# Kernel tuning notes

Hardware: AMD Instinct MI355X
Metric: run time of the kernel (lower is better)

## Reference

```python
import jax, jax.numpy as jnp
import numpy as np

L, D, H, F, K = 2, 256, 8, 512, 9
M, G1, G2, NT = 4, 40, 40, 2048
DH = D // H
KPD = 3  # per-dim neighbour window; KPD**2 == K


def setup_inputs() -> dict:
    key = jax.random.key(0)
    ks = jax.random.split(key, 16)
    s = 0.02
    ax0 = jnp.linspace(-1.0, 1.0, G1)
    ax1 = jnp.linspace(-1.0, 1.0, G2)
    gx, gy = jnp.meshgrid(ax0, ax1, indexing='ij')
    xc = jnp.broadcast_to(jnp.stack([gx, gy], -1), (M, G1, G2, 2))  # regular grid coords
    zc = jax.random.normal(ks[0], (M, G1, G2, D), dtype=jnp.float32)
    xt = jax.random.uniform(ks[1], (M, NT, 2), minval=-1.0, maxval=1.0)
    zt = jax.random.normal(ks[2], (M, NT, D), dtype=jnp.float32)
    def n(k, shape):
        return jax.random.normal(k, shape, dtype=jnp.float32) * s
    def ln():
        return jnp.stack([jnp.ones((L, D)), jnp.zeros((L, D))], 1)  # [L, 2(gamma,beta), D]
    return dict(
        xc=xc, zc=zc, xt=xt, zt=zt,
        sa_wqkv=n(ks[3], (L, D, 3 * D)), sa_wo=n(ks[4], (L, D, D)),
        sa_ln1=ln(), sa_ln2=ln(),
        sa_w1=n(ks[5], (L, D, F)), sa_b1=jnp.zeros((L, F)),
        sa_w2=n(ks[6], (L, F, D)), sa_b2=jnp.zeros((L, D)),
        ca_wq=n(ks[7], (L, D, D)), ca_wkv=n(ks[8], (L, D, 2 * D)), ca_wo=n(ks[9], (L, D, D)),
        ca_lnq=ln(), ca_lnkv=ln(), ca_ln2=ln(),
        ca_w1=n(ks[10], (L, D, F)), ca_b1=jnp.zeros((L, F)),
        ca_w2=n(ks[11], (L, F, D)), ca_b2=jnp.zeros((L, D)),
    )


def _ln(x, p):
    mu = x.mean(-1, keepdims=True)
    var = ((x - mu) ** 2).mean(-1, keepdims=True)
    return (x - mu) * jax.lax.rsqrt(var + 1e-5) * p[0] + p[1]


def nearest_gridded_neighbours(xt, xc):
    """Separable per-dim nearest grid index + KPD x KPD window, clamped at borders.
    Returns flat neighbour indices [M, NT, K] and validity mask [M, NT, K]."""
    ax0 = xc[:, :, 0, 0]  # [M, G1] axis-0 coordinates
    ax1 = xc[:, 0, :, 1]  # [M, G2] axis-1 coordinates
    n0 = jnp.argmin(jnp.abs(xt[..., 0:1] - ax0[:, None, :]), -1)  # [M, NT]
    n1 = jnp.argmin(jnp.abs(xt[..., 1:2] - ax1[:, None, :]), -1)
    off = jnp.arange(KPD) - KPD // 2
    r0 = n0[..., None] + off  # [M, NT, KPD]
    r1 = n1[..., None] + off
    v0 = (r0 >= 0) & (r0 < G1)
    v1 = (r1 >= 0) & (r1 < G2)
    i0 = jnp.clip(r0, 0, G1 - 1)
    i1 = jnp.clip(r1, 0, G2 - 1)
    idx = (i0[:, :, :, None] * G2 + i1[:, :, None, :]).reshape(xt.shape[0], -1, K)
    mask = (v0[:, :, :, None] & v1[:, :, None, :]).reshape(xt.shape[0], -1, K)
    return idx, mask


def reference(xc, zc, xt, zt, sa_wqkv, sa_wo, sa_ln1, sa_ln2, sa_w1, sa_b1, sa_w2, sa_b2,
              ca_wq, ca_wkv, ca_wo, ca_lnq, ca_lnkv, ca_ln2, ca_w1, ca_b1, ca_w2, ca_b2):
    m = zc.shape[0]
    idx, mask = nearest_gridded_neighbours(xt, xc)
    zc = zc.reshape(m, G1 * G2, D)  # flatten_grid
    bidx = jnp.arange(m)[:, None, None]
    scale = 1.0 / np.sqrt(DH)
    for l in range(L):
        # --- MHSA over flattened grid (pre-norm transformer block) ---
        h = _ln(zc, sa_ln1[l])
        q, k, v = jnp.split(h @ sa_wqkv[l], 3, -1)
        q = q.reshape(m, -1, H, DH); k = k.reshape(m, -1, H, DH); v = v.reshape(m, -1, H, DH)
        att = jax.nn.softmax(jnp.einsum('bnhd,bkhd->bhnk', q, k) * scale, -1)
        o = jnp.einsum('bhnk,bkhd->bnhd', att, v).reshape(m, -1, D)
        zc = zc + o @ sa_wo[l]
        h = _ln(zc, sa_ln2[l])
        zc = zc + jax.nn.gelu(h @ sa_w1[l] + sa_b1[l]) @ sa_w2[l] + sa_b2[l]
        # --- per-target masked MHCA over K nearest grid tokens (MATH SDPA path) ---
        nzc = zc[bidx, idx]  # [M, NT, K, D] neighbour gather
        q = (_ln(zt, ca_lnq[l]) @ ca_wq[l]).reshape(m, NT, H, DH)
        kk, vv = jnp.split(_ln(nzc, ca_lnkv[l]) @ ca_wkv[l], 2, -1)
        kk = kk.reshape(m, NT, K, H, DH); vv = vv.reshape(m, NT, K, H, DH)
        s = jnp.einsum('bnhd,bnkhd->bnhk', q, kk) * scale
        s = jnp.where(mask[:, :, None, :], s, -1e30)
        att = jax.nn.softmax(s, -1)
        o = jnp.einsum('bnhk,bnkhd->bnhd', att, vv).reshape(m, NT, D)
        zt = zt + o @ ca_wo[l]
        h = _ln(zt, ca_ln2[l])
        zt = zt + jax.nn.gelu(h @ ca_w1[l] + ca_b1[l]) @ ca_w2[l] + ca_b2[l]
    return zt
```

## Files before the change

kernel.cpp:

```cpp
#include <hip/hip_runtime.h>
#include <math.h>

#define LAYERS 2
#define DMODEL 256
#define NHEAD  8
#define DHEAD  32
#define FF     512
#define KNB    9
#define MB     4
#define G1D    40
#define G2D    40
#define NTGT   2048
#define NCTX   1600
#define RC     (MB*NCTX)
#define RT     (MB*NTGT)
#define NSPLIT 4

typedef __attribute__((ext_vector_type(8))) short short8;
typedef __attribute__((ext_vector_type(4))) float f32x4;

#if __has_builtin(__builtin_amdgcn_exp2f)
#define EXP2(x) __builtin_amdgcn_exp2f(x)
#else
#define EXP2(x) exp2f(x)
#endif
#define L2E 1.4426950408889634f
#define ATTN_SCALE 0.17677669529663687f

#define ZC_OFF    0
#define HC_OFF    1638400
#define HT_OFF    (HC_OFF + 819200)
#define QKV_OFF   (HC_OFF + 2097152)
#define WT_OFF    (QKV_OFF + 3400000)
#define FB_OFF    (QKV_OFF + 4500000)
#define Q_OFF     (QKV_OFF + 4915200)
#define O_OFF     (Q_OFF + 2097152)
#define IDX_OFF   (O_OFF + 2097152)
#define MASK_OFF  (IDX_OFF + 73728)
#define OPART_OFF (MASK_OFF + 73728)
#define LB_OFF    (OPART_OFF + 3276800)
#define WS_FLOATS (LB_OFF + 204800)

#define WT_LAYER   1048576
#define WT_QKV     0
#define WT_WO      196608
#define WT_W1      262144
#define WT_W2      393216
#define WT_CWQ     524288
#define WT_CWKV    589824
#define WT_CWO     720896
#define WT_CW1     786432
#define WT_CW2     917504
#define FB_LAYER   2560
#define FB_QKV     0
#define FB_W1      768
#define FB_WKV     1280
#define FB_WQ      1792
#define FB_CW1     2048

static __device__ __forceinline__ float gelu_f(float x){
  float t = tanhf(0.7978845608028654f * (x + 0.044715f * x * x * x));
  return 0.5f * x * (1.0f + t);
}
static __device__ __forceinline__ unsigned int bf16_rne(float x){
  unsigned int u = __float_as_uint(x);
  return (u + 0x7fffu + ((u >> 16) & 1u)) >> 16;
}
static __device__ __forceinline__ unsigned int pack_bf16x2(float lo, float hi){
  return bf16_rne(lo) | (bf16_rne(hi) << 16);
}
static __device__ __forceinline__ float bfu(unsigned int u16){
  return __uint_as_float(u16 << 16);
}

struct TDesc { const float* src; const float* gamma; int dstoff; int K; int N; int nse; float nsc; };
struct TTable { TDesc e[18]; };

__global__ __launch_bounds__(256)
void wprep_kernel(TTable t, unsigned short* __restrict__ wt){
  TDesc d = t.e[blockIdx.z];
  int n0 = blockIdx.x * 32, k0 = blockIdx.y * 32;
  if (n0 >= d.N || k0 >= d.K) return;
  __shared__ float tile[32][33];
  int tx = threadIdx.x, ty = threadIdx.y;
  float csc = (n0 + tx < d.nse) ? d.nsc : 1.0f;
  #pragma unroll
  for (int j = 0; j < 4; j++){
    int k = k0 + ty * 4 + j;
    float v = d.src[(size_t)k * d.N + n0 + tx];
    if (d.gamma) v *= d.gamma[k];
    tile[ty * 4 + j][tx] = v * csc;
  }
  __syncthreads();
  #pragma unroll
  for (int j = 0; j < 4; j++)
    wt[(size_t)d.dstoff + (size_t)(n0 + ty * 4 + j) * d.K + k0 + tx] =
        (unsigned short)bf16_rne(tile[tx][ty * 4 + j]);
}

struct BDesc { const float* W; const float* beta; const float* base; int outoff; int N; int nse; float nsc; };
struct BTable { BDesc e[10]; };

__global__ __launch_bounds__(256)
void bfold_kernel(BTable t, float* __restrict__ fb){
  BDesc d = t.e[blockIdx.x];
  int n = blockIdx.y * 64 + (threadIdx.x >> 2);
  int q = threadIdx.x & 3;
  if (n >= d.N) return;
  float s = 0.f;
  #pragma unroll 4
  for (int k = q * 64; k < q * 64 + 64; k++)
    s += d.beta[k] * d.W[(size_t)k * d.N + n];
  s += __shfl_xor(s, 1);
  s += __shfl_xor(s, 2);
  if (q == 0){
    float r = s + (d.base ? d.base[n] : 0.f);
    if (n < d.nse) r *= d.nsc;
    fb[d.outoff + n] = r;
  }
}

__global__ void nn_idx_kernel(const float* __restrict__ xc, const float* __restrict__ xt,
                              int* __restrict__ idx, float* __restrict__ mask){
  int g = blockIdx.x * blockDim.x + threadIdx.x;
  if (g >= MB * NTGT) return;
  int m = g >> 11;
  float x0 = xt[(size_t)g * 2 + 0];
  float x1 = xt[(size_t)g * 2 + 1];
  const float* xcm = xc + (size_t)m * G1D * G2D * 2;
  int n0 = 0; float b0 = 1e30f;
  for (int i = 0; i < G1D; i++){
    float d = fabsf(x0 - xcm[i * (G2D * 2)]);
    if (d < b0){ b0 = d; n0 = i; }
  }
  int n1 = 0; float b1 = 1e30f;
  for (int j = 0; j < G2D; j++){
    float d = fabsf(x1 - xcm[j * 2 + 1]);
    if (d < b1){ b1 = d; n1 = j; }
  }
  #pragma unroll
  for (int a = 0; a < 3; a++){
    int r0 = n0 + a - 1;
    bool v0 = (r0 >= 0) && (r0 < G1D);
    int i0 = min(max(r0, 0), G1D - 1);
    #pragma unroll
    for (int b = 0; b < 3; b++){
      int r1 = n1 + b - 1;
      bool v1 = (r1 >= 0) && (r1 < G2D);
      int i1 = min(max(r1, 0), G2D - 1);
      idx [(size_t)g * KNB + a * 3 + b] = i0 * G2D + i1;
      mask[(size_t)g * KNB + a * 3 + b] = (v0 && v1) ? 1.0f : 0.0f;
    }
  }
}

__global__ __launch_bounds__(256)
void ln_norm(const float* __restrict__ x, unsigned short* __restrict__ y, int rows){
  int gw   = blockIdx.x * 4 + (threadIdx.x >> 6);
  int lane = threadIdx.x & 63;
  if (gw >= rows) return;
  const float* xr = x + (size_t)gw * DMODEL;
  int d0 = lane * 4;
  float4 xv = *(const float4*)(xr + d0);
  float s = xv.x + xv.y + xv.z + xv.w;
  #pragma unroll
  for (int off = 32; off > 0; off >>= 1) s += __shfl_xor(s, off);
  float mu = s * (1.0f / DMODEL);
  float dx0 = xv.x - mu, dx1 = xv.y - mu, dx2 = xv.z - mu, dx3 = xv.w - mu;
  float v = dx0*dx0 + dx1*dx1 + dx2*dx2 + dx3*dx3;
  #pragma unroll
  for (int off = 32; off > 0; off >>= 1) v += __shfl_xor(v, off);
  float rs = rsqrtf(v * (1.0f / DMODEL) + 1e-5f);
  uint2 w;
  w.x = pack_bf16x2(dx0 * rs, dx1 * rs);
  w.y = pack_bf16x2(dx2 * rs, dx3 * rs);
  *(uint2*)(y + (size_t)gw * DMODEL + d0) = w;
}

template<int ROWS>
static __device__ __forceinline__ void stage_glds(const unsigned short* __restrict__ src,
                                                  int Ksrc, unsigned short* lds,
                                                  int wave, int lane){
  #pragma unroll
  for (int j = 0; j < ROWS / 32; j++){
    int ublk = (j * 4 + wave) * 64;
    int u    = ublk + lane;
    int row  = u >> 3;
    int unit = (u & 7) ^ (row & 7);
    __builtin_amdgcn_global_load_lds(
        (const __attribute__((address_space(1))) void*)(src + (size_t)row * Ksrc + unit * 8),
        (__attribute__((address_space(3))) void*)(lds + (size_t)ublk * 8),
        16, 0, 0);
  }
}

template<int K, int MT, int NT>
__global__ __launch_bounds__(256)
void gemm_glds(const unsigned short* __restrict__ A, const unsigned short* __restrict__ Wt,
               const float* __restrict__ bias, const float* __restrict__ res,
               void* __restrict__ C, int N, int flags){
  const int MFR = MT / 32, NFR = NT / 32;
  __shared__ unsigned short Als[2][MT * 64];
  __shared__ unsigned short Bls[2][NT * 64];
  int tid = threadIdx.x;
  int wave = tid >> 6, lane = tid & 63;
  int wm = wave >> 1, wn = wave & 1;
  int l16 = lane & 15, grp = lane >> 4;
  int r0 = blockIdx.y * MT, c0 = blockIdx.x * NT;

  const unsigned short* Ag = A  + (size_t)r0 * K;
  const unsigned short* Bg = Wt + (size_t)c0 * K;
  const int nch = K >> 6;

  stage_glds<MT>(Ag, K, Als[0], wave, lane);
  stage_glds<NT>(Bg, K, Bls[0], wave, lane);

  f32x4 acc[MFR][NFR];
  #pragma unroll
  for (int m = 0; m < MFR; m++)
    #pragma unroll
    for (int n = 0; n < NFR; n++) acc[m][n] = (f32x4){0.f, 0.f, 0.f, 0.f};

  #pragma unroll
  for (int ch = 0; ch < nch; ch++){
    int b = ch & 1;
    __syncthreads();
    if (ch + 1 < nch){
      stage_glds<MT>(Ag + (ch + 1) * 64, K, Als[b ^ 1], wave, lane);
      stage_glds<NT>(Bg + (ch + 1) * 64, K, Bls[b ^ 1], wave, lane);
    }
    const unsigned short* Ab = Als[b];
    const unsigned short* Bb = Bls[b];
    #pragma unroll
    for (int kk = 0; kk < 2; kk++){
      short8 af[MFR], bfr[NFR];
      #pragma unroll
      for (int m = 0; m < MFR; m++){
        int row = wm * (MT / 2) + m * 16 + l16;
        int unit = (kk * 4 + grp) ^ (row & 7);
        af[m] = *(const short8*)(Ab + row * 64 + unit * 8);
      }
      #pragma unroll
      for (int n = 0; n < NFR; n++){
        int row = wn * (NT / 2) + n * 16 + l16;
        int unit = (kk * 4 + grp) ^ (row & 7);
        bfr[n] = *(const short8*)(Bb + row * 64 + unit * 8);
      }
      #pragma unroll
      for (int m = 0; m < MFR; m++)
        #pragma unroll
        for (int n = 0; n < NFR; n++)
          acc[m][n] = __builtin_amdgcn_mfma_f32_16x16x32_bf16(af[m], bfr[n], acc[m][n], 0, 0, 0);
    }
  }

  #pragma unroll
  for (int n = 0; n < NFR; n++){
    int gc = c0 + wn * (NT / 2) + n * 16 + l16;
    float bv = (flags & 1) ? bias[gc] : 0.f;
    #pragma unroll
    for (int m = 0; m < MFR; m++){
      int grb = r0 + wm * (MT / 2) + m * 16 + grp * 4;
      #pragma unroll
      for (int r = 0; r < 4; r++){
        float v = acc[m][n][r] + bv;
        if (flags & 2) v = gelu_f(v);
        if (flags & 4) v += res[(size_t)(grb + r) * N + gc];
        if (flags & 8) ((unsigned short*)C)[(size_t)(grb + r) * N + gc] = (unsigned short)bf16_rne(v);
        else           ((float*)C)[(size_t)(grb + r) * N + gc] = v;
      }
    }
  }
}

#define KSTR 40
#define VSTR 70
#define PSTR 72
__global__ __launch_bounds__(256)
void sa_attn_mfma(const unsigned short* __restrict__ qkv,
                  unsigned short* __restrict__ opart, float* __restrict__ lb){
  int mz = blockIdx.z;
  int m = mz & 3, split = mz >> 2;
  int h = blockIdx.y;
  int tid  = threadIdx.x;
  int wave = tid >> 6, lane = tid & 63;
  int qr = lane & 15, grp = lane >> 4;
  int q0 = blockIdx.x * 64 + wave * 16;

  int kt0 = split ? (7 + (split - 1) * 6) : 0;
  int kt1 = kt0 + (split ? 6 : 7);

  __shared__ unsigned short Kls[2][64 * KSTR];
  __shared__ unsigned short Vls[2][32 * VSTR];
  __shared__ unsigned short Pls[4][16 * PSTR];
  unsigned short* Pw = Pls[wave];

  short8 qf = *(const short8*)(qkv + ((size_t)(m * NCTX + q0 + qr)) * 768 + h * 32 + grp * 8);

  int skey = tid >> 2;
  int scol = (tid & 3) * 8;
  const unsigned short* kbase = qkv + (size_t)m * NCTX * 768 + 256 + h * 32 + scol;

  uint4 kreg = *(const uint4*)(kbase + (size_t)(kt0 * 64 + skey) * 768);
  uint4 vreg = *(const uint4*)(kbase + (size_t)(kt0 * 64 + skey) * 768 + 256);

  float lq = 0.0f;
  f32x4 acc0 = {0.f, 0.f, 0.f, 0.f};
  f32x4 acc1 = {0.f, 0.f, 0.f, 0.f};

  {
    *(uint4*)&Kls[0][skey * KSTR + scol] = kreg;
    unsigned int vv[4] = {vreg.x, vreg.y, vreg.z, vreg.w};
    #pragma unroll
    for (int j = 0; j < 4; j++){
      Vls[0][(scol + 2 * j    ) * VSTR + skey] = (unsigned short)(vv[j] & 0xffffu);
      Vls[0][(scol + 2 * j + 1) * VSTR + skey] = (unsigned short)(vv[j] >> 16);
    }
  }

  for (int kt = kt0; kt < kt1; kt++){
    int b = (kt - kt0) & 1;
    __syncthreads();
    if (kt + 1 < kt1){
      kreg = *(const uint4*)(kbase + (size_t)((kt + 1) * 64 + skey) * 768);
      vreg = *(const uint4*)(kbase + (size_t)((kt + 1) * 64 + skey) * 768 + 256);
    }

    f32x4 s0 = {0.f,0.f,0.f,0.f}, s1 = {0.f,0.f,0.f,0.f};
    f32x4 s2 = {0.f,0.f,0.f,0.f}, s3 = {0.f,0.f,0.f,0.f};
    {
      const short8 k0 = *(const short8*)&Kls[b][( 0 + qr) * KSTR + grp * 8];
      const short8 k1 = *(const short8*)&Kls[b][(16 + qr) * KSTR + grp * 8];
      const short8 k2 = *(const short8*)&Kls[b][(32 + qr) * KSTR + grp * 8];
      const short8 k3 = *(const short8*)&Kls[b][(48 + qr) * KSTR + grp * 8];
      s0 = __builtin_amdgcn_mfma_f32_16x16x32_bf16(k0, qf, s0, 0, 0, 0);
      s1 = __builtin_amdgcn_mfma_f32_16x16x32_bf16(k1, qf, s1, 0, 0, 0);
      s2 = __builtin_amdgcn_mfma_f32_16x16x32_bf16(k2, qf, s2, 0, 0, 0);
      s3 = __builtin_amdgcn_mfma_f32_16x16x32_bf16(k3, qf, s3, 0, 0, 0);
    }

    float p[4][4];
    #pragma unroll
    for (int r = 0; r < 4; r++){
      p[0][r] = EXP2(s0[r]); p[1][r] = EXP2(s1[r]);
      p[2][r] = EXP2(s2[r]); p[3][r] = EXP2(s3[r]);
    }
    #pragma unroll
    for (int kb = 0; kb < 4; kb++)
      #pragma unroll
      for (int r = 0; r < 4; r++) lq += p[kb][r];

    #pragma unroll
    for (int kb = 0; kb < 4; kb++){
      *(unsigned int*)&Pw[qr * PSTR + kb * 16 + grp * 4]     = pack_bf16x2(p[kb][0], p[kb][1]);
      *(unsigned int*)&Pw[qr * PSTR + kb * 16 + grp * 4 + 2] = pack_bf16x2(p[kb][2], p[kb][3]);
    }

    #pragma unroll
    for (int hh = 0; hh < 2; hh++){
      const short8 pf = *(const short8*)&Pw[qr * PSTR + hh * 32 + grp * 8];
      const short8 v0 = *(const short8*)&Vls[b][( 0 + qr) * VSTR + hh * 32 + grp * 8];
      const short8 v1 = *(const short8*)&Vls[b][(16 + qr) * VSTR + hh * 32 + grp * 8];
      acc0 = __builtin_amdgcn_mfma_f32_16x16x32_bf16(v0, pf, acc0, 0, 0, 0);
      acc1 = __builtin_amdgcn_mfma_f32_16x16x32_bf16(v1, pf, acc1, 0, 0, 0);
    }

    if (kt + 1 < kt1){
      *(uint4*)&Kls[b ^ 1][skey * KSTR + scol] = kreg;
      unsigned int vv[4] = {vreg.x, vreg.y, vreg.z, vreg.w};
      #pragma unroll
      for (int j = 0; j < 4; j++){
        Vls[b ^ 1][(scol + 2 * j    ) * VSTR + skey] = (unsigned short)(vv[j] & 0xffffu);
        Vls[b ^ 1][(scol + 2 * j + 1) * VSTR + skey] = (unsigned short)(vv[j] >> 16);
      }
    }
  }

  lq += __shfl_xor(lq, 16);
  lq += __shfl_xor(lq, 32);
  float inv = 1.0f / lq;
  int gr = m * NCTX + q0 + qr;
  unsigned short* op = opart + ((size_t)(split * RC + gr)) * DMODEL + h * DHEAD;
  uint2 o16a, o16b;
  o16a.x = pack_bf16x2(acc0[0] * inv, acc0[1] * inv);
  o16a.y = pack_bf16x2(acc0[2] * inv, acc0[3] * inv);
  o16b.x = pack_bf16x2(acc1[0] * inv, acc1[1] * inv);
  o16b.y = pack_bf16x2(acc1[2] * inv, acc1[3] * inv);
  *(uint2*)(op + grp * 4)      = o16a;
  *(uint2*)(op + 16 + grp * 4) = o16b;
  if (grp == 0)
    lb[((size_t)(split * RC + gr)) * 8 + h] = lq;
}

__global__ __launch_bounds__(256)
void sa_merge(const unsigned short* __restrict__ opart, const float* __restrict__ lb,
              unsigned short* __restrict__ out){
  int g = blockIdx.x * 256 + threadIdx.x;
  int gr = g >> 6;
  int d4 = (g & 63) * 4;
  int h  = d4 >> 5;
  float l[NSPLIT];
  float lsum = 0.f;
  #pragma unroll
  for (int s = 0; s < NSPLIT; s++){
    l[s] = lb[(size_t)(s * RC + gr) * 8 + h];
    lsum += l[s];
  }
  float inv = 1.0f / lsum;
  float o0 = 0.f, o1 = 0.f, o2 = 0.f, o3 = 0.f;
  #pragma unroll
  for (int s = 0; s < NSPLIT; s++){
    float w = l[s] * inv;
    uint2 a = *(const uint2*)(opart + (size_t)(s * RC + gr) * DMODEL + d4);
    o0 += bfu(a.x & 0xffffu) * w;
    o1 += bfu(a.x >> 16)     * w;
    o2 += bfu(a.y & 0xffffu) * w;
    o3 += bfu(a.y >> 16)     * w;
  }
  uint2 w;
  w.x = pack_bf16x2(o0, o1);
  w.y = pack_bf16x2(o2, o3);
  *(uint2*)(out + (size_t)gr * DMODEL + d4) = w;
}

__global__ __launch_bounds__(256)
void ca_attn_kernel(const float* __restrict__ qb, const float* __restrict__ kv,
                    const int* __restrict__ idx, const float* __restrict__ mask,
                    unsigned short* __restrict__ ob){
  int g = blockIdx.x;
  int m = g >> 11;
  int tid = threadIdx.x;
  float q = qb[(size_t)g * DMODEL + tid];
  float s[KNB];
  int rws[KNB];
  #pragma unroll
  for (int k = 0; k < KNB; k++){
    int row = idx[(size_t)g * KNB + k];
    rws[k] = row;
    float p = q * kv[((size_t)(m * NCTX + row)) * 512 + tid];
    #pragma unroll
    for (int off = 16; off > 0; off >>= 1) p += __shfl_xor(p, off, 32);
    s[k] = (mask[(size_t)g * KNB + k] > 0.5f) ? p : -1e30f;
  }
  float sm = s[0];
  #pragma unroll
  for (int k = 1; k < KNB; k++) sm = fmaxf(sm, s[k]);
  float den = 0.f, w[KNB];
  #pragma unroll
  for (int k = 0; k < KNB; k++){ w[k] = __expf(s[k] - sm); den += w[k]; }
  float inv = 1.0f / den;
  float o = 0.f;
  #pragma unroll
  for (int k = 0; k < KNB; k++)
    o += w[k] * kv[((size_t)(m * NCTX + rws[k])) * 512 + 256 + tid];
  ob[(size_t)g * DMODEL + tid] = (unsigned short)bf16_rne(o * inv);
}

static inline void launch_gemm(const unsigned short* A, const unsigned short* Wt,
                               const float* bias, const float* res, void* C,
                               int R, int K, int N, int flags, hipStream_t stream){
  if (N == 768){
    gemm_glds<256, 64, 128><<<dim3(N / 128, R / 64), 256, 0, stream>>>(A, Wt, bias, res, C, N, flags);
  } else if (K == 256){
    gemm_glds<256, 64, 64><<<dim3(N / 64, R / 64), 256, 0, stream>>>(A, Wt, bias, res, C, N, flags);
  } else {
    gemm_glds<512, 64, 64><<<dim3(N / 64, R / 64), 256, 0, stream>>>(A, Wt, bias, res, C, N, flags);
  }
}

extern "C" void kernel_launch(void* const* d_in, const int* in_sizes, int n_in,
                              void* d_out, int out_size, void* d_ws, size_t ws_size,
                              hipStream_t stream){
  const float* xc      = (const float*)d_in[0];
  const float* zc_in   = (const float*)d_in[1];
  const float* xt      = (const float*)d_in[2];
  const float* zt_in   = (const float*)d_in[3];
  const float* sa_wqkv = (const float*)d_in[4];
  const float* sa_wo   = (const float*)d_in[5];
  const float* sa_ln1  = (const float*)d_in[6];
  const float* sa_ln2  = (const float*)d_in[7];
  const float* sa_w1   = (const float*)d_in[8];
  const float* sa_b1   = (const float*)d_in[9];
  const float* sa_w2   = (const float*)d_in[10];
  const float* sa_b2   = (const float*)d_in[11];
  const float* ca_wq   = (const float*)d_in[12];
  const float* ca_wkv  = (const float*)d_in[13];
  const float* ca_wo   = (const float*)d_in[14];
  const float* ca_lnq  = (const float*)d_in[15];
  const float* ca_lnkv = (const float*)d_in[16];
  const float* ca_ln2  = (const float*)d_in[17];
  const float* ca_w1   = (const float*)d_in[18];
  const float* ca_b1   = (const float*)d_in[19];
  const float* ca_w2   = (const float*)d_in[20];
  const float* ca_b2   = (const float*)d_in[21];

  if (ws_size < (size_t)WS_FLOATS * sizeof(float)) return;
  float* ws    = (float*)d_ws;
  float* zc    = ws + ZC_OFF;
  unsigned short* hc16 = (unsigned short*)(ws + HC_OFF);
  unsigned short* ht16 = (unsigned short*)(ws + HT_OFF);
  float* qkvb  = ws + QKV_OFF;
  unsigned short* qkv16 = (unsigned short*)qkvb;
  unsigned short* wt    = (unsigned short*)(ws + WT_OFF);
  float* fb    = ws + FB_OFF;
  float* qb    = ws + Q_OFF;
  unsigned short* ob16    = (unsigned short*)(ws + O_OFF);
  unsigned short* opart16 = (unsigned short*)(ws + OPART_OFF);
  float* lbuf  = ws + LB_OFF;
  int*   idxb  = (int*)(ws + IDX_OFF);
  float* maskb = ws + MASK_OFF;
  float* zt    = (float*)d_out;

  const float QSC = ATTN_SCALE * L2E;

  TTable tt;
  for (int l = 0; l < LAYERS; l++){
    int b = l * WT_LAYER, i = l * 9;
    tt.e[i + 0] = { sa_wqkv + (size_t)l * 256 * 768, sa_ln1  + l * 512, b + WT_QKV,  256, 768, 256, QSC };
    tt.e[i + 1] = { sa_wo   + (size_t)l * 256 * 256, nullptr,           b + WT_WO,   256, 256, 0, 1.f };
    tt.e[i + 2] = { sa_w1   + (size_t)l * 256 * 512, sa_ln2  + l * 512, b + WT_W1,   256, 512, 0, 1.f };
    tt.e[i + 3] = { sa_w2   + (size_t)l * 512 * 256, nullptr,           b + WT_W2,   512, 256, 0, 1.f };
    tt.e[i + 4] = { ca_wq   + (size_t)l * 256 * 256, ca_lnq  + l * 512, b + WT_CWQ,  256, 256, 256, ATTN_SCALE };
    tt.e[i + 5] = { ca_wkv  + (size_t)l * 256 * 512, ca_lnkv + l * 512, b + WT_CWKV, 256, 512, 0, 1.f };
    tt.e[i + 6] = { ca_wo   + (size_t)l * 256 * 256, nullptr,           b + WT_CWO,  256, 256, 0, 1.f };
    tt.e[i + 7] = { ca_w1   + (size_t)l * 256 * 512, ca_ln2  + l * 512, b + WT_CW1,  256, 512, 0, 1.f };
    tt.e[i + 8] = { ca_w2   + (size_t)l * 512 * 256, nullptr,           b + WT_CW2,  512, 256, 0, 1.f };
  }
  wprep_kernel<<<dim3(24, 16, 18), dim3(32, 8), 0, stream>>>(tt, wt);

  BTable bt;
  for (int l = 0; l < LAYERS; l++){
    int fo = l * FB_LAYER, i = l * 5;
    bt.e[i + 0] = { sa_wqkv + (size_t)l * 256 * 768, sa_ln1  + l * 512 + 256, nullptr,        fo + FB_QKV, 768, 256, QSC };
    bt.e[i + 1] = { sa_w1   + (size_t)l * 256 * 512, sa_ln2  + l * 512 + 256, sa_b1 + l * FF, fo + FB_W1,  512, 0, 1.f };
    bt.e[i + 2] = { ca_wkv  + (size_t)l * 256 * 512, ca_lnkv + l * 512 + 256, nullptr,        fo + FB_WKV, 512, 0, 1.f };
    bt.e[i + 3] = { ca_wq   + (size_t)l * 256 * 256, ca_lnq  + l * 512 + 256, nullptr,        fo + FB_WQ,  256, 256, ATTN_SCALE };
    bt.e[i + 4] = { ca_w1   + (size_t)l * 256 * 512, ca_ln2  + l * 512 + 256, ca_b1 + l * FF, fo + FB_CW1, 512, 0, 1.f };
  }
  bfold_kernel<<<dim3(10, 12), 256, 0, stream>>>(bt, fb);

  nn_idx_kernel<<<(MB * NTGT) / 256, 256, 0, stream>>>(xc, xt, idxb, maskb);

  ln_norm<<<RC / 4, 256, 0, stream>>>(zc_in, hc16, RC);

  for (int l = 0; l < LAYERS; l++){
    const unsigned short* wl = wt + (size_t)l * WT_LAYER;
    const float* fl = fb + (size_t)l * FB_LAYER;
    const float* zc_src = (l == 0) ? zc_in : zc;
    const float* zt_src = (l == 0) ? zt_in : zt;

    launch_gemm(hc16, wl + WT_QKV, fl + FB_QKV, nullptr, qkv16, RC, 256, 768, 1 | 8, stream);
    sa_attn_mfma<<<dim3(NCTX / 64, NHEAD, MB * NSPLIT), 256, 0, stream>>>(qkv16, opart16, lbuf);
    sa_merge<<<RC * 64 / 256, 256, 0, stream>>>(opart16, lbuf, ht16);
    launch_gemm(ht16, wl + WT_WO, nullptr, zc_src, zc, RC, 256, 256, 4, stream);
    ln_norm<<<RC / 4, 256, 0, stream>>>(zc, hc16, RC);
    launch_gemm(hc16, wl + WT_W1, fl + FB_W1, nullptr, qkv16, RC, 256, 512, 1 | 2 | 8, stream);
    launch_gemm(qkv16, wl + WT_W2, sa_b2 + l * DMODEL, zc, zc, RC, 512, 256, 1 | 4, stream);

    ln_norm<<<RC / 4, 256, 0, stream>>>(zc, hc16, RC);
    launch_gemm(hc16, wl + WT_CWKV, fl + FB_WKV, nullptr, qkvb, RC, 256, 512, 1, stream);
    ln_norm<<<RT / 4, 256, 0, stream>>>(zt_src, ht16, RT);
    launch_gemm(ht16, wl + WT_CWQ, fl + FB_WQ, nullptr, qb, RT, 256, 256, 1, stream);
    ca_attn_kernel<<<RT, 256, 0, stream>>>(qb, qkvb, idxb, maskb, ob16);
    launch_gemm(ob16, wl + WT_CWO, nullptr, zt_src, zt, RT, 256, 256, 4, stream);
    ln_norm<<<RT / 4, 256, 0, stream>>>(zt, ht16, RT);
    launch_gemm(ht16, wl + WT_CW1, fl + FB_CW1, nullptr, qkv16, RT, 256, 512, 1 | 2 | 8, stream);
    launch_gemm(qkv16, wl + WT_CW2, ca_b2 + l * DMODEL, zt, zt, RT, 512, 256, 1 | 4, stream);
  }
}
```

Measured before the change: 368.9 us.

## Fuse split-attention merge into Wo GEMM and batch CA LN/projection launches

Measured after the change: 392.4 us. +6.4%, slower.

```diff
diff --git a/kernel.cpp b/kernel.cpp
--- a/kernel.cpp
+++ b/kernel.cpp
@@ -154,12 +154,8 @@
   }
 }
 
-__global__ __launch_bounds__(256)
-void ln_norm(const float* __restrict__ x, unsigned short* __restrict__ y, int rows){
-  int gw   = blockIdx.x * 4 + (threadIdx.x >> 6);
-  int lane = threadIdx.x & 63;
-  if (gw >= rows) return;
-  const float* xr = x + (size_t)gw * DMODEL;
+static __device__ __forceinline__ void ln_row(const float* __restrict__ xr,
+                                              unsigned short* __restrict__ yr, int lane){
   int d0 = lane * 4;
   float4 xv = *(const float4*)(xr + d0);
   float s = xv.x + xv.y + xv.z + xv.w;
@@ -174,7 +170,28 @@
   uint2 w;
   w.x = pack_bf16x2(dx0 * rs, dx1 * rs);
   w.y = pack_bf16x2(dx2 * rs, dx3 * rs);
-  *(uint2*)(y + (size_t)gw * DMODEL + d0) = w;
+  *(uint2*)(yr + d0) = w;
+}
+
+__global__ __launch_bounds__(256)
+void ln_norm(const float* __restrict__ x, unsigned short* __restrict__ y, int rows){
+  int gw   = blockIdx.x * 4 + (threadIdx.x >> 6);
+  int lane = threadIdx.x & 63;
+  if (gw >= rows) return;
+  ln_row(x + (size_t)gw * DMODEL, y + (size_t)gw * DMODEL, lane);
+}
+
+__global__ __launch_bounds__(256)
+void ln_norm2(const float* __restrict__ xa, unsigned short* __restrict__ ya, int ra,
+              const float* __restrict__ xb, unsigned short* __restrict__ yb){
+  int gw   = blockIdx.x * 4 + (threadIdx.x >> 6);
+  int lane = threadIdx.x & 63;
+  if (gw < ra)
+    ln_row(xa + (size_t)gw * DMODEL, ya + (size_t)gw * DMODEL, lane);
+  else {
+    int g2 = gw - ra;
+    ln_row(xb + (size_t)g2 * DMODEL, yb + (size_t)g2 * DMODEL, lane);
+  }
 }
 
 template<int ROWS>
@@ -269,6 +286,192 @@
         if (flags & 8) ((unsigned short*)C)[(size_t)(grb + r) * N + gc] = (unsigned short)bf16_rne(v);
         else           ((float*)C)[(size_t)(grb + r) * N + gc] = v;
       }
+    }
+  }
+}
+
+__global__ __launch_bounds__(256)
+void gemm_womerge(const unsigned short* __restrict__ opart, const float* __restrict__ lb,
+                  const unsigned short* __restrict__ Wt, const float* __restrict__ res,
+                  float* __restrict__ C){
+  __shared__ unsigned short Als[64 * 256];
+  __shared__ unsigned short Bls[2][64 * 64];
+  int tid = threadIdx.x;
+  int wave = tid >> 6, lane = tid & 63;
+  int wm = wave >> 1, wn = wave & 1;
+  int l16 = lane & 15, grp = lane >> 4;
+  int r0 = blockIdx.y * 64, c0 = blockIdx.x * 64;
+
+  const unsigned short* Bg = Wt + (size_t)c0 * 256;
+  stage_glds<64>(Bg, 256, Bls[0], wave, lane);
+
+  {
+    int row = tid >> 2;
+    int cseg = (tid & 3) * 64;
+    int gr = r0 + row;
+    int h0 = cseg >> 5;
+    float w0[NSPLIT], w1[NSPLIT];
+    float ls0 = 0.f, ls1 = 0.f;
+    #pragma unroll
+    for (int s = 0; s < NSPLIT; s++){
+      w0[s] = lb[(size_t)(s * RC + gr) * 8 + h0];
+      w1[s] = lb[(size_t)(s * RC + gr) * 8 + h0 + 1];
+      ls0 += w0[s]; ls1 += w1[s];
+    }
+    float i0 = 1.0f / ls0, i1 = 1.0f / ls1;
+    #pragma unroll
+    for (int s = 0; s < NSPLIT; s++){ w0[s] *= i0; w1[s] *= i1; }
+
+    #pragma unroll
+    for (int u = 0; u < 8; u++){
+      int gcol = cseg + u * 8;
+      const float* w = (u < 4) ? w0 : w1;
+      float o[8] = {0,0,0,0,0,0,0,0};
+      #pragma unroll
+      for (int s = 0; s < NSPLIT; s++){
+        short8 a = *(const short8*)(opart + (size_t)(s * RC + gr) * DMODEL + gcol);
+        float ws = w[s];
+        #pragma unroll
+        for (int j = 0; j < 8; j++)
+          o[j] += bfu((unsigned short)a[j]) * ws;
+      }
+      short8 sv;
+      #pragma unroll
+      for (int j = 0; j < 8; j++) sv[j] = (short)bf16_rne(o[j]);
+      int gu = gcol >> 3;
+      int slot = (gu & ~7) | ((gu & 7) ^ (row & 7));
+      *(short8*)&Als[row * 256 + slot * 8] = sv;
+    }
+  }
+
+  f32x4 acc[2][2];
+  #pragma unroll
+  for (int m = 0; m < 2; m++)
+    #pragma unroll
+    for (int n = 0; n < 2; n++) acc[m][n] = (f32x4){0.f, 0.f, 0.f, 0.f};
+
+  #pragma unroll
+  for (int ch = 0; ch < 4; ch++){
+    int b = ch & 1;
+    __syncthreads();
+    if (ch + 1 < 4)
+      stage_glds<64>(Bg + (ch + 1) * 64, 256, Bls[b ^ 1], wave, lane);
+    const unsigned short* Bb = Bls[b];
+    #pragma unroll
+    for (int kk = 0; kk < 2; kk++){
+      short8 af[2], bfr[2];
+      #pragma unroll
+      for (int m = 0; m < 2; m++){
+        int row = wm * 32 + m * 16 + l16;
+        int slot = ch * 8 + ((kk * 4 + grp) ^ (row & 7));
+        af[m] = *(const short8*)(Als + row * 256 + slot * 8);
+      }
+      #pragma unroll
+      for (int n = 0; n < 2; n++){
+        int row = wn * 32 + n * 16 + l16;
+        int unit = (kk * 4 + grp) ^ (row & 7);
+        bfr[n] = *(const short8*)(Bb + row * 64 + unit * 8);
+      }
+      #pragma unroll
+      for (int m = 0; m < 2; m++)
+        #pragma unroll
+        for (int n = 0; n < 2; n++)
+          acc[m][n] = __builtin_amdgcn_mfma_f32_16x16x32_bf16(af[m], bfr[n], acc[m][n], 0, 0, 0);
+    }
+  }
+
+  #pragma unroll
+  for (int n = 0; n < 2; n++){
+    int gc = c0 + wn * 32 + n * 16 + l16;
+    #pragma unroll
+    for (int m = 0; m < 2; m++){
+      int grb = r0 + wm * 32 + m * 16 + grp * 4;
+      #pragma unroll
+      for (int r = 0; r < 4; r++){
+        float v = acc[m][n][r] + res[(size_t)(grb + r) * 256 + gc];
+        C[(size_t)(grb + r) * 256 + gc] = v;
+      }
+    }
+  }
+}
+
+__global__ __launch_bounds__(256)
+void gemm_wkvq(const unsigned short* __restrict__ A0, const unsigned short* __restrict__ W0,
+               const float* __restrict__ b0, float* __restrict__ C0,
+               const unsigned short* __restrict__ A1, const unsigned short* __restrict__ W1,
+               const float* __restrict__ b1, float* __restrict__ C1){
+  int z = blockIdx.z;
+  int N = z ? 256 : 512;
+  int R = z ? RT : RC;
+  if ((int)blockIdx.x * 64 >= N || (int)blockIdx.y * 64 >= R) return;
+  const unsigned short* A  = z ? A1 : A0;
+  const unsigned short* Wt = z ? W1 : W0;
+  const float* bias        = z ? b1 : b0;
+  float* C                 = z ? C1 : C0;
+
+  __shared__ unsigned short Als[2][64 * 64];
+  __shared__ unsigned short Bls[2][64 * 64];
+  int tid = threadIdx.x;
+  int wave = tid >> 6, lane = tid & 63;
+  int wm = wave >> 1, wn = wave & 1;
+  int l16 = lane & 15, grp = lane >> 4;
+  int r0 = blockIdx.y * 64, c0 = blockIdx.x * 64;
+
+  const unsigned short* Ag = A  + (size_t)r0 * 256;
+  const unsigned short* Bg = Wt + (size_t)c0 * 256;
+
+  stage_glds<64>(Ag, 256, Als[0], wave, lane);
+  stage_glds<64>(Bg, 256, Bls[0], wave, lane);
+
+  f32x4 acc[2][2];
+  #pragma unroll
+  for (int m = 0; m < 2; m++)
+    #pragma unroll
+    for (int n = 0; n < 2; n++) acc[m][n] = (f32x4){0.f, 0.f, 0.f, 0.f};
+
+  #pragma unroll
+  for (int ch = 0; ch < 4; ch++){
+    int b = ch & 1;
+    __syncthreads();
+    if (ch + 1 < 4){
+      stage_glds<64>(Ag + (ch + 1) * 64, 256, Als[b ^ 1], wave, lane);
+      stage_glds<64>(Bg + (ch + 1) * 64, 256, Bls[b ^ 1], wave, lane);
+    }
+    const unsigned short* Ab = Als[b];
+    const unsigned short* Bb = Bls[b];
+    #pragma unroll
+    for (int kk = 0; kk < 2; kk++){
+      short8 af[2], bfr[2];
+      #pragma unroll
+      for (int m = 0; m < 2; m++){
+        int row = wm * 32 + m * 16 + l16;
+        int unit = (kk * 4 + grp) ^ (row & 7);
+        af[m] = *(const short8*)(Ab + row * 64 + unit * 8);
+      }
+      #pragma unroll
+      for (int n = 0; n < 2; n++){
+        int row = wn * 32 + n * 16 + l16;
+        int unit = (kk * 4 + grp) ^ (row & 7);
+        bfr[n] = *(const short8*)(Bb + row * 64 + unit * 8);
+      }
+      #pragma unroll
+      for (int m = 0; m < 2; m++)
+        #pragma unroll
+        for (int n = 0; n < 2; n++)
+          acc[m][n] = __builtin_amdgcn_mfma_f32_16x16x32_bf16(af[m], bfr[n], acc[m][n], 0, 0, 0);
+    }
+  }
+
+  #pragma unroll
+  for (int n = 0; n < 2; n++){
+    int gc = c0 + wn * 32 + n * 16 + l16;
+    float bv = bias[gc];
+    #pragma unroll
+    for (int m = 0; m < 2; m++){
+      int grb = r0 + wm * 32 + m * 16 + grp * 4;
+      #pragma unroll
+      for (int r = 0; r < 4; r++)
+        C[(size_t)(grb + r) * N + gc] = acc[m][n][r] + bv;
     }
   }
 }
@@ -390,37 +593,6 @@
   *(uint2*)(op + 16 + grp * 4) = o16b;
   if (grp == 0)
     lb[((size_t)(split * RC + gr)) * 8 + h] = lq;
-}
-
-__global__ __launch_bounds__(256)
-void sa_merge(const unsigned short* __restrict__ opart, const float* __restrict__ lb,
-              unsigned short* __restrict__ out){
-  int g = blockIdx.x * 256 + threadIdx.x;
-  int gr = g >> 6;
-  int d4 = (g & 63) * 4;
-  int h  = d4 >> 5;
-  float l[NSPLIT];
-  float lsum = 0.f;
-  #pragma unroll
-  for (int s = 0; s < NSPLIT; s++){
-    l[s] = lb[(size_t)(s * RC + gr) * 8 + h];
-    lsum += l[s];
-  }
-  float inv = 1.0f / lsum;
-  float o0 = 0.f, o1 = 0.f, o2 = 0.f, o3 = 0.f;
-  #pragma unroll
-  for (int s = 0; s < NSPLIT; s++){
-    float w = l[s] * inv;
-    uint2 a = *(const uint2*)(opart + (size_t)(s * RC + gr) * DMODEL + d4);
-    o0 += bfu(a.x & 0xffffu) * w;
-    o1 += bfu(a.x >> 16)     * w;
-    o2 += bfu(a.y & 0xffffu) * w;
-    o3 += bfu(a.y >> 16)     * w;
-  }
-  uint2 w;
-  w.x = pack_bf16x2(o0, o1);
-  w.y = pack_bf16x2(o2, o3);
-  *(uint2*)(out + (size_t)gr * DMODEL + d4) = w;
 }
 
 __global__ __launch_bounds__(256)
@@ -551,16 +723,15 @@
 
     launch_gemm(hc16, wl + WT_QKV, fl + FB_QKV, nullptr, qkv16, RC, 256, 768, 1 | 8, stream);
     sa_attn_mfma<<<dim3(NCTX / 64, NHEAD, MB * NSPLIT), 256, 0, stream>>>(qkv16, opart16, lbuf);
-    sa_merge<<<RC * 64 / 256, 256, 0, stream>>>(opart16, lbuf, ht16);
-    launch_gemm(ht16, wl + WT_WO, nullptr, zc_src, zc, RC, 256, 256, 4, stream);
+    gemm_womerge<<<dim3(4, RC / 64), 256, 0, stream>>>(opart16, lbuf, wl + WT_WO, zc_src, zc);
     ln_norm<<<RC / 4, 256, 0, stream>>>(zc, hc16, RC);
     launch_gemm(hc16, wl + WT_W1, fl + FB_W1, nullptr, qkv16, RC, 256, 512, 1 | 2 | 8, stream);
     launch_gemm(qkv16, wl + WT_W2, sa_b2 + l * DMODEL, zc, zc, RC, 512, 256, 1 | 4, stream);
 
-    ln_norm<<<RC / 4, 256, 0, stream>>>(zc, hc16, RC);
-    launch_gemm(hc16, wl + WT_CWKV, fl + FB_WKV, nullptr, qkvb, RC, 256, 512, 1, stream);
-    ln_norm<<<RT / 4, 256, 0, stream>>>(zt_src, ht16, RT);
-    launch_gemm(ht16, wl + WT_CWQ, fl + FB_WQ, nullptr, qb, RT, 256, 256, 1, stream);
+    ln_norm2<<<(RC + RT) / 4, 256, 0, stream>>>(zc, hc16, RC, zt_src, ht16);
+    gemm_wkvq<<<dim3(8, RT / 64, 2), 256, 0, stream>>>(
+        hc16, wl + WT_CWKV, fl + FB_WKV, qkvb,
+        ht16, wl + WT_CWQ,  fl + FB_WQ,  qb);
     ca_attn_kernel<<<RT, 256, 0, stream>>>(qb, qkvb, idxb, maskb, ob16);
     launch_gemm(ob16, wl + WT_CWO, nullptr, zt_src, zt, RT, 256, 256, 4, stream);
     ln_norm<<<RT / 4, 256, 0, stream>>>(zt, ht16, RT);
```
